# Performance work log

Hardware: AMD Instinct MI355X
Metric: run time of the kernel (lower is better)

## Reference

```python
import jax, jax.numpy as jnp
import numpy as np

D_MODEL = 1024
N_HEADS = 16
HEAD_DIM = D_MODEL // N_HEADS


def setup_inputs() -> dict:
    key = jax.random.key(0)
    kx, kq, kk, kv, ko = jax.random.split(key, 5)
    scale = 1.0 / np.sqrt(D_MODEL)
    x = jax.random.normal(kx, (4, 2048, D_MODEL), dtype=jnp.float32)
    # nn.Linear weights stored as [out, in]; y = x @ W.T
    W_q = jax.random.normal(kq, (D_MODEL, D_MODEL), dtype=jnp.float32) * scale
    W_k = jax.random.normal(kk, (D_MODEL, D_MODEL), dtype=jnp.float32) * scale
    W_v = jax.random.normal(kv, (D_MODEL, D_MODEL), dtype=jnp.float32) * scale
    W_o = jax.random.normal(ko, (D_MODEL, D_MODEL), dtype=jnp.float32) * scale
    return {"x": x, "W_q": W_q, "W_k": W_k, "W_v": W_v, "W_o": W_o}


def reference(x, W_q, W_k, W_v, W_o):
    B, T, C = x.shape
    H, Dh = N_HEADS, HEAD_DIM

    def proj(W):
        return (x @ W.T).reshape(B, T, H, Dh).transpose(0, 2, 1, 3)  # [B,H,T,Dh]

    Q = proj(W_q)
    K = proj(W_q)  # faithful to source bug: K uses W_q, W_k is unused
    V = proj(W_v)

    scores = jnp.einsum('bhqd,bhkd->bhqk', Q, K) / np.sqrt(Dh)
    causal = jnp.tril(jnp.ones((T, T), dtype=bool))
    scores = jnp.where(causal, scores, -jnp.inf)
    attn = jax.nn.softmax(scores, axis=-1)
    out = jnp.einsum('bhqk,bhkd->bhqd', attn, V)
    out = out.transpose(0, 2, 1, 3).reshape(B, T, C)
    return out @ W_o.T
```

## Files before the change

kernel.cpp:

```cpp
#include <hip/hip_runtime.h>
#include <hip/hip_bf16.h>
#include <type_traits>

typedef unsigned short u16;
typedef __attribute__((ext_vector_type(8))) short bf16x8;
typedef __attribute__((ext_vector_type(4))) float f32x4;
typedef __attribute__((ext_vector_type(2))) unsigned int u32x2;

#define B_  4
#define T_  2048
#define C_  1024
#define H_  16
#define DH_ 64
#define M_  (B_*T_)

#define GLDS16(g, l) __builtin_amdgcn_global_load_lds( \
    (const __attribute__((address_space(1))) void*)(g), \
    (__attribute__((address_space(3))) void*)(l), 16, 0, 0)

__device__ __forceinline__ u16 f2b(float f) {
  union { __hip_bfloat16 h; u16 u; } cv;
  cv.h = __float2bfloat16(f);
  return cv.u;
}

__global__ void cast_all_kernel(const float* __restrict__ x,  const float* __restrict__ w0,
                                const float* __restrict__ w1, const float* __restrict__ w2,
                                u16* __restrict__ xo, u16* __restrict__ o0,
                                u16* __restrict__ o1, u16* __restrict__ o2) {
  int bid = blockIdx.x;
  const float* src; u16* dst; int blk;
  if (bid < 8192) { src = x; dst = xo; blk = bid; }
  else {
    int k = bid - 8192, w = k >> 10;
    src = (w == 0) ? w0 : (w == 1) ? w1 : w2;
    dst = (w == 0) ? o0 : (w == 1) ? o1 : o2;
    blk = k & 1023;
  }
  int i = (blk * 256 + threadIdx.x) * 4;
  float4 v = *(const float4*)(src + i);
  unsigned lo = (unsigned)f2b(v.x) | ((unsigned)f2b(v.y) << 16);
  unsigned hi = (unsigned)f2b(v.z) | ((unsigned)f2b(v.w) << 16);
  uint2 p; p.x = lo; p.y = hi;
  *(uint2*)(dst + i) = p;
}

__global__ __launch_bounds__(256) void gemm_bt_kernel(
    const u16* __restrict__ A, const u16* __restrict__ Bm,
    void* __restrict__ Cout, int mode)
{
  constexpr int K = 1024;
  __shared__ __align__(16) u16 As[128 * 64];
  __shared__ __align__(16) u16 Bs[128 * 64];

  const int tid  = threadIdx.x;
  const int wave = tid >> 6, lane = tid & 63;
  const int quad = lane >> 4, l15 = lane & 15;
  const int x7   = l15 & 7;
  const int wm = (wave >> 1) * 64, wn = (wave & 1) * 64;
  const int tm = blockIdx.x * 128, tn = blockIdx.y * 128;

  f32x4 acc[4][4] = {};

  for (int k0 = 0; k0 < K; k0 += 64) {
#pragma unroll
    for (int it = 0; it < 4; it++) {
      int ch  = it * 256 + tid;
      int row = ch >> 3;
      int cc  = (ch & 7) ^ (row & 7);
      GLDS16(A  + (size_t)(tm + row) * K + k0 + cc * 8, &As[(it * 256 + wave * 64) * 8]);
      GLDS16(Bm + (size_t)(tn + row) * K + k0 + cc * 8, &Bs[(it * 256 + wave * 64) * 8]);
    }
    __syncthreads();

#pragma unroll
    for (int ks = 0; ks < 2; ks++) {
      bf16x8 af[4], bfr[4];
#pragma unroll
      for (int t = 0; t < 4; t++) {
        int co = ((ks * 4 + quad) ^ x7) * 8;
        af[t]  = *(const bf16x8*)(&As[(wm + t * 16 + l15) * 64 + co]);
        bfr[t] = *(const bf16x8*)(&Bs[(wn + t * 16 + l15) * 64 + co]);
      }
#pragma unroll
      for (int mt = 0; mt < 4; mt++)
#pragma unroll
        for (int nt = 0; nt < 4; nt++)
          acc[mt][nt] = __builtin_amdgcn_mfma_f32_16x16x32_bf16(af[mt], bfr[nt], acc[mt][nt], 0, 0, 0);
    }
    __syncthreads();
  }

  if (mode == 0) {
    u16* out = (u16*)Cout;
    if (tn < 1024) {
#pragma unroll
      for (int mt = 0; mt < 4; mt++)
#pragma unroll
        for (int nt = 0; nt < 4; nt++)
#pragma unroll
          for (int r = 0; r < 4; r++) {
            int gm = tm + wm + mt * 16 + quad * 4 + r;
            int gn = tn + wn + nt * 16 + l15;
            int b = gm >> 11, t = gm & 2047;
            int h = gn >> 6, d = gn & 63;
            out[((size_t)((b * 16 + h) * 2048 + t) << 6) + d] = f2b(acc[mt][nt][r]);
          }
    } else {
#pragma unroll
      for (int mt = 0; mt < 4; mt++)
#pragma unroll
        for (int nt = 0; nt < 4; nt++) {
          int gm0 = tm + wm + mt * 16 + quad * 4;
          int gn  = tn - 1024 + wn + nt * 16 + l15;
          int b = gm0 >> 11, t0 = gm0 & 2047;
          int h = gn >> 6, d = gn & 63;
          alignas(8) u16 tmp[4];
#pragma unroll
          for (int r = 0; r < 4; r++) tmp[r] = f2b(acc[mt][nt][r]);
          *(ushort4*)(out + 8388608 + (((size_t)(b * 16 + h) * 64 + d) << 11) + t0)
              = *(const ushort4*)tmp;
        }
    }
  } else {
    float* out = (float*)Cout;
#pragma unroll
    for (int mt = 0; mt < 4; mt++)
#pragma unroll
      for (int nt = 0; nt < 4; nt++)
#pragma unroll
        for (int r = 0; r < 4; r++) {
          int gm = tm + wm + mt * 16 + quad * 4 + r;
          int gn = tn + wn + nt * 16 + l15;
          out[(size_t)gm * 1024 + gn] = acc[mt][nt][r];
        }
  }
}

__global__ __launch_bounds__(512, 4) void gemm_bt512_kernel(
    const u16* __restrict__ A, const u16* __restrict__ Bm, float* __restrict__ out)
{
  constexpr int K = 1024;
  __shared__ __align__(16) u16 As[128 * 64];
  __shared__ __align__(16) u16 Bs[128 * 64];

  const int tid  = threadIdx.x;
  const int wave = tid >> 6, lane = tid & 63;
  const int quad = lane >> 4, l15 = lane & 15;
  const int x7   = l15 & 7;
  const int wm = (wave >> 1) * 32, wn = (wave & 1) * 64;
  const int tm = blockIdx.x * 128, tn = blockIdx.y * 128;

  f32x4 acc[2][4] = {};

  for (int k0 = 0; k0 < K; k0 += 64) {
#pragma unroll
    for (int it = 0; it < 2; it++) {
      int ch  = it * 512 + tid;
      int row = ch >> 3;
      int cc  = (ch & 7) ^ (row & 7);
      GLDS16(A  + (size_t)(tm + row) * K + k0 + cc * 8, &As[(it * 512 + wave * 64) * 8]);
      GLDS16(Bm + (size_t)(tn + row) * K + k0 + cc * 8, &Bs[(it * 512 + wave * 64) * 8]);
    }
    __syncthreads();

#pragma unroll
    for (int ks = 0; ks < 2; ks++) {
      bf16x8 af[2], bfr[4];
      int co = ((ks * 4 + quad) ^ x7) * 8;
#pragma unroll
      for (int t = 0; t < 2; t++)
        af[t]  = *(const bf16x8*)(&As[(wm + t * 16 + l15) * 64 + co]);
#pragma unroll
      for (int t = 0; t < 4; t++)
        bfr[t] = *(const bf16x8*)(&Bs[(wn + t * 16 + l15) * 64 + co]);
#pragma unroll
      for (int mt = 0; mt < 2; mt++)
#pragma unroll
        for (int nt = 0; nt < 4; nt++)
          acc[mt][nt] = __builtin_amdgcn_mfma_f32_16x16x32_bf16(af[mt], bfr[nt], acc[mt][nt], 0, 0, 0);
    }
    __syncthreads();
  }

#pragma unroll
  for (int mt = 0; mt < 2; mt++)
#pragma unroll
    for (int nt = 0; nt < 4; nt++)
#pragma unroll
      for (int r = 0; r < 4; r++) {
        int gm = tm + wm + mt * 16 + quad * 4 + r;
        int gn = tn + wn + nt * 16 + l15;
        out[(size_t)gm * 1024 + gn] = acc[mt][nt][r];
      }
}

__global__ __launch_bounds__(256, 4) void attn_kernel(
    const u16* __restrict__ Q, const u16* __restrict__ Vt, u16* __restrict__ AO)
{
  __shared__ __align__(16) u16 Ks[2][4096];
  __shared__ __align__(16) u16 Vs[2][4096];

  const int tid  = threadIdx.x;
  const int wave = tid >> 6, lane = tid & 63;
  const int quad = lane >> 4, l15 = lane & 15;
  const int x7   = l15 & 7;
  const int krow = (l15 & 3) | ((l15 & 4) << 1) | ((l15 & 8) >> 1);
  const int kx7  = krow & 7;
  const int bid  = blockIdx.x;
  const int bh = (bid & 7) * 8 + ((bid >> 3) & 7);
  const int m  = bid >> 6;
  const int i  = (m & 4) ? ((m & 8) ? m - 12 : m + 4) : 15 - m;
  const int b = bh >> 4, h = bh & 15;
  const u16* Qbh = Q  + (size_t)bh * (T_ * DH_);
  const u16* Vbh = Vt + (size_t)bh * (DH_ * T_);
  const int q0w = i * 128 + wave * 32;
  const int kbd = (q0w + 31) >> 6;
  const int nkb = 2 * i + 2;

  const float C1 = 0.18033688f;
  const float C2 = -28.8539008f;
  const bf16x8 ones = { 0x3F80, 0x3F80, 0x3F80, 0x3F80, 0x3F80, 0x3F80, 0x3F80, 0x3F80 };

  f32x4 o[2][4] = {};
  f32x4 lsumv[2] = {};

  auto stage = [&](int kb, int bufi) {
    const int k0 = kb * 64;
#pragma unroll
    for (int it = 0; it < 2; it++) {
      int ch  = it * 256 + tid;
      int row = ch >> 3;
      int cc  = (ch & 7) ^ (row & 7);
      GLDS16(Qbh + (size_t)(k0 + row) * DH_ + cc * 8, &Ks[bufi][(it * 256 + wave * 64) * 8]);
      GLDS16(Vbh + (size_t)row * T_ + k0 + cc * 8,    &Vs[bufi][(it * 256 + wave * 64) * 8]);
    }
  };

  stage(0, 0);

  bf16x8 qf[2][2];
#pragma unroll
  for (int mt = 0; mt < 2; mt++)
#pragma unroll
    for (int ks = 0; ks < 2; ks++)
      qf[mt][ks] = *(const bf16x8*)(Qbh + (size_t)(q0w + mt * 16 + l15) * DH_ + ks * 32 + quad * 8);

  auto tilecomp = [&](int kb, int bufi, auto DIAGC) {
    constexpr bool DIAG = decltype(DIAGC)::value;
    const int k0 = kb * 64;
    const u16* KsB = Ks[bufi];
    const u16* VsB = Vs[bufi];

    f32x4 s[2][4] = {};
#pragma unroll
    for (int ks = 0; ks < 2; ks++)
#pragma unroll
      for (int nt = 0; nt < 4; nt++) {
        bf16x8 kf = *(const bf16x8*)(&KsB[(nt * 16 + krow) * 64 + (((ks * 4 + quad) ^ kx7) * 8)]);
#pragma unroll
        for (int mt = 0; mt < 2; mt++)
          s[mt][nt] = __builtin_amdgcn_mfma_f32_16x16x32_bf16(kf, qf[mt][ks], s[mt][nt], 0, 0, 0);
      }

    unsigned c[2][4][2];
#pragma unroll
    for (int mt = 0; mt < 2; mt++)
#pragma unroll
      for (int nt = 0; nt < 4; nt++) {
        u16 pb[4];
#pragma unroll
        for (int r = 0; r < 4; r++) {
          float p = __builtin_amdgcn_exp2f(s[mt][nt][r] * C1 + C2);
          if constexpr (DIAG) {
            int qg = q0w + mt * 16 + l15;
            int kg = k0 + nt * 16 + (quad & 1) * 8 + (quad >> 1) * 4 + r;
            p = (kg <= qg) ? p : 0.0f;
          }
          pb[r] = f2b(p);
        }
        c[mt][nt][0] = (unsigned)pb[0] | ((unsigned)pb[1] << 16);
        c[mt][nt][1] = (unsigned)pb[2] | ((unsigned)pb[3] << 16);
      }

#pragma unroll
    for (int ks2 = 0; ks2 < 2; ks2++) {
      bf16x8 pf[2];
#pragma unroll
      for (int mt = 0; mt < 2; mt++) {
        u32x2 w02 = __builtin_amdgcn_permlane32_swap(c[mt][2 * ks2][0], c[mt][2 * ks2 + 1][0], false, false);
        u32x2 w13 = __builtin_amdgcn_permlane32_swap(c[mt][2 * ks2][1], c[mt][2 * ks2 + 1][1], false, false);
        union { unsigned u[4]; bf16x8 v; } pk;
        pk.u[0] = w02[0]; pk.u[1] = w13[0]; pk.u[2] = w02[1]; pk.u[3] = w13[1];
        pf[mt] = pk.v;
        lsumv[mt] = __builtin_amdgcn_mfma_f32_16x16x32_bf16(pf[mt], ones, lsumv[mt], 0, 0, 0);
      }
#pragma unroll
      for (int dt = 0; dt < 4; dt++) {
        bf16x8 vf = *(const bf16x8*)(&VsB[(dt * 16 + l15) * 64 + (((ks2 * 4 + quad) ^ x7) * 8)]);
#pragma unroll
        for (int mt = 0; mt < 2; mt++)
          o[mt][dt] = __builtin_amdgcn_mfma_f32_16x16x32_bf16(pf[mt], vf, o[mt][dt], 0, 0, 0);
      }
    }
  };

  for (int kb = 0; kb < nkb; kb++) {
    __syncthreads();
    if (kb + 1 < nkb) stage(kb + 1, (kb + 1) & 1);
    const int bufi = kb & 1;
    if (kb < kbd)        tilecomp(kb, bufi, std::false_type{});
    else if (kb == kbd)  tilecomp(kb, bufi, std::true_type{});
  }

#pragma unroll
  for (int mt = 0; mt < 2; mt++)
#pragma unroll
    for (int r = 0; r < 4; r++) {
      float rl = 1.0f / lsumv[mt][r];
      int t = q0w + mt * 16 + quad * 4 + r;
#pragma unroll
      for (int dt = 0; dt < 4; dt++)
        AO[((size_t)(b * T_ + t)) * C_ + h * DH_ + dt * 16 + l15] = f2b(o[mt][dt][r] * rl);
    }
}

extern "C" void kernel_launch(void* const* d_in, const int* in_sizes, int n_in,
                              void* d_out, int out_size, void* d_ws, size_t ws_size,
                              hipStream_t stream) {
  (void)in_sizes; (void)n_in; (void)out_size; (void)ws_size;
  const float* x  = (const float*)d_in[0];
  const float* Wq = (const float*)d_in[1];
  const float* Wv = (const float*)d_in[3];
  const float* Wo = (const float*)d_in[4];

  u16* Xb  = (u16*)d_ws;
  u16* AOw = Xb;
  u16* Wqb = Xb  + 8388608;
  u16* Wvb = Wqb + 1048576;
  u16* Wob = Wvb + 1048576;
  u16* Qw  = Wob + 1048576;
  u16* Vtw = Qw  + 8388608;

  cast_all_kernel<<<11264, 256, 0, stream>>>(x, Wq, Wv, Wo, Xb, Wqb, Wvb, Wob);

  gemm_bt_kernel<<<dim3(64, 16), 256, 0, stream>>>(Xb, Wqb, (void*)Qw, 0);

  attn_kernel<<<1024, 256, 0, stream>>>(Qw, Vtw, AOw);

  gemm_bt512_kernel<<<dim3(64, 8), 512, 0, stream>>>(AOw, Wob, (float*)d_out);
}
```

Baseline: 210.3 us.

## Replace GEMMs with 256x128-tile multi-buffered pipelined kernel using manual waitcnt

Both projection GEMMs now use one templated kernel with 512 threads and 256x128 output tiles. It triple-buffers the A tile and double-buffers the B tile in LDS, prefetching future K slices with global_load_lds and waiting on partial vmcnt counts, so loads overlap MFMA work instead of hitting a full sync on every iteration. The larger tiles raise operand reuse and halve the block count. The cost is more LDS per block, lower occupancy, and fewer blocks for the output GEMM, which launches only 256.

```diff
diff --git a/kernel.cpp b/kernel.cpp
--- a/kernel.cpp
+++ b/kernel.cpp
@@ -45,53 +45,86 @@
   *(uint2*)(dst + i) = p;
 }
 
-__global__ __launch_bounds__(256) void gemm_bt_kernel(
-    const u16* __restrict__ A, const u16* __restrict__ Bm,
-    void* __restrict__ Cout, int mode)
+template<int MODE>
+__global__ __launch_bounds__(512, 2) void gemm256_kernel(
+    const u16* __restrict__ A, const u16* __restrict__ Bm, void* __restrict__ Cout)
 {
   constexpr int K = 1024;
-  __shared__ __align__(16) u16 As[128 * 64];
-  __shared__ __align__(16) u16 Bs[128 * 64];
+  constexpr int NT = K / 64;
+  __shared__ __align__(16) u16 As[3][256 * 64];
+  __shared__ __align__(16) u16 Bs[2][128 * 64];
 
   const int tid  = threadIdx.x;
   const int wave = tid >> 6, lane = tid & 63;
   const int quad = lane >> 4, l15 = lane & 15;
   const int x7   = l15 & 7;
-  const int wm = (wave >> 1) * 64, wn = (wave & 1) * 64;
-  const int tm = blockIdx.x * 128, tn = blockIdx.y * 128;
+  const int wr = wave >> 1, wc = wave & 1;
+  const int tm = blockIdx.x * 256, tn = blockIdx.y * 128;
 
   f32x4 acc[4][4] = {};
 
-  for (int k0 = 0; k0 < K; k0 += 64) {
+  auto stageA = [&](int t, int bi) {
+    const int k0 = t * 64;
 #pragma unroll
     for (int it = 0; it < 4; it++) {
-      int ch  = it * 256 + tid;
+      int ch  = it * 512 + tid;
       int row = ch >> 3;
       int cc  = (ch & 7) ^ (row & 7);
-      GLDS16(A  + (size_t)(tm + row) * K + k0 + cc * 8, &As[(it * 256 + wave * 64) * 8]);
-      GLDS16(Bm + (size_t)(tn + row) * K + k0 + cc * 8, &Bs[(it * 256 + wave * 64) * 8]);
-    }
-    __syncthreads();
-
-#pragma unroll
-    for (int ks = 0; ks < 2; ks++) {
-      bf16x8 af[4], bfr[4];
-#pragma unroll
-      for (int t = 0; t < 4; t++) {
-        int co = ((ks * 4 + quad) ^ x7) * 8;
-        af[t]  = *(const bf16x8*)(&As[(wm + t * 16 + l15) * 64 + co]);
-        bfr[t] = *(const bf16x8*)(&Bs[(wn + t * 16 + l15) * 64 + co]);
-      }
+      GLDS16(A + (size_t)(tm + row) * K + k0 + cc * 8, &As[bi][(it * 512 + wave * 64) * 8]);
+    }
+  };
+  auto stageB = [&](int t, int bi) {
+    const int k0 = t * 64;
+#pragma unroll
+    for (int it = 0; it < 2; it++) {
+      int ch  = it * 512 + tid;
+      int row = ch >> 3;
+      int cc  = (ch & 7) ^ (row & 7);
+      GLDS16(Bm + (size_t)(tn + row) * K + k0 + cc * 8, &Bs[bi][(it * 512 + wave * 64) * 8]);
+    }
+  };
+
+  stageB(0, 0);
+  stageA(0, 0);
+  stageA(1, 1);
+
+  int bufA = 0, bufAn = 2;
+  for (int t = 0; t < NT; t++) {
+    __builtin_amdgcn_s_barrier();
+    if (t + 1 < NT) stageB(t + 1, (t + 1) & 1);
+    if (t + 2 < NT) { stageA(t + 2, bufAn); bufAn = (bufAn == 2) ? 0 : bufAn + 1; }
+    if (t < NT - 2)       asm volatile("s_waitcnt vmcnt(10)" ::: "memory");
+    else if (t == NT - 2) asm volatile("s_waitcnt vmcnt(6)"  ::: "memory");
+    else                  asm volatile("s_waitcnt vmcnt(0)"  ::: "memory");
+    __builtin_amdgcn_sched_barrier(0);
+    __builtin_amdgcn_s_barrier();
+    __builtin_amdgcn_sched_barrier(0);
+
+    const u16* Ab = &As[bufA][0];
+    const u16* Bb = &Bs[t & 1][0];
+    bufA = (bufA == 2) ? 0 : bufA + 1;
+
+    bf16x8 af[4][2], bfr[4][2];
+#pragma unroll
+    for (int mt = 0; mt < 4; mt++)
+#pragma unroll
+      for (int ks = 0; ks < 2; ks++)
+        af[mt][ks] = *(const bf16x8*)(&Ab[(wr * 64 + mt * 16 + l15) * 64 + (((ks * 4 + quad) ^ x7) * 8)]);
+#pragma unroll
+    for (int nt = 0; nt < 4; nt++)
+#pragma unroll
+      for (int ks = 0; ks < 2; ks++)
+        bfr[nt][ks] = *(const bf16x8*)(&Bb[(wc * 64 + nt * 16 + l15) * 64 + (((ks * 4 + quad) ^ x7) * 8)]);
+#pragma unroll
+    for (int ks = 0; ks < 2; ks++)
 #pragma unroll
       for (int mt = 0; mt < 4; mt++)
 #pragma unroll
         for (int nt = 0; nt < 4; nt++)
-          acc[mt][nt] = __builtin_amdgcn_mfma_f32_16x16x32_bf16(af[mt], bfr[nt], acc[mt][nt], 0, 0, 0);
-    }
-    __syncthreads();
+          acc[mt][nt] = __builtin_amdgcn_mfma_f32_16x16x32_bf16(af[mt][ks], bfr[nt][ks], acc[mt][nt], 0, 0, 0);
   }
 
-  if (mode == 0) {
+  if constexpr (MODE == 0) {
     u16* out = (u16*)Cout;
     if (tn < 1024) {
 #pragma unroll
@@ -100,8 +133,8 @@
         for (int nt = 0; nt < 4; nt++)
 #pragma unroll
           for (int r = 0; r < 4; r++) {
-            int gm = tm + wm + mt * 16 + quad * 4 + r;
-            int gn = tn + wn + nt * 16 + l15;
+            int gm = tm + wr * 64 + mt * 16 + quad * 4 + r;
+            int gn = tn + wc * 64 + nt * 16 + l15;
             int b = gm >> 11, t = gm & 2047;
             int h = gn >> 6, d = gn & 63;
             out[((size_t)((b * 16 + h) * 2048 + t) << 6) + d] = f2b(acc[mt][nt][r]);
@@ -111,8 +144,8 @@
       for (int mt = 0; mt < 4; mt++)
 #pragma unroll
         for (int nt = 0; nt < 4; nt++) {
-          int gm0 = tm + wm + mt * 16 + quad * 4;
-          int gn  = tn - 1024 + wn + nt * 16 + l15;
+          int gm0 = tm + wr * 64 + mt * 16 + quad * 4;
+          int gn  = tn - 1024 + wc * 64 + nt * 16 + l15;
           int b = gm0 >> 11, t0 = gm0 & 2047;
           int h = gn >> 6, d = gn & 63;
           alignas(8) u16 tmp[4];
@@ -130,69 +163,11 @@
       for (int nt = 0; nt < 4; nt++)
 #pragma unroll
         for (int r = 0; r < 4; r++) {
-          int gm = tm + wm + mt * 16 + quad * 4 + r;
-          int gn = tn + wn + nt * 16 + l15;
+          int gm = tm + wr * 64 + mt * 16 + quad * 4 + r;
+          int gn = tn + wc * 64 + nt * 16 + l15;
           out[(size_t)gm * 1024 + gn] = acc[mt][nt][r];
         }
   }
-}
-
-__global__ __launch_bounds__(512, 4) void gemm_bt512_kernel(
-    const u16* __restrict__ A, const u16* __restrict__ Bm, float* __restrict__ out)
-{
-  constexpr int K = 1024;
-  __shared__ __align__(16) u16 As[128 * 64];
-  __shared__ __align__(16) u16 Bs[128 * 64];
-
-  const int tid  = threadIdx.x;
-  const int wave = tid >> 6, lane = tid & 63;
-  const int quad = lane >> 4, l15 = lane & 15;
-  const int x7   = l15 & 7;
-  const int wm = (wave >> 1) * 32, wn = (wave & 1) * 64;
-  const int tm = blockIdx.x * 128, tn = blockIdx.y * 128;
-
-  f32x4 acc[2][4] = {};
-
-  for (int k0 = 0; k0 < K; k0 += 64) {
-#pragma unroll
-    for (int it = 0; it < 2; it++) {
-      int ch  = it * 512 + tid;
-      int row = ch >> 3;
-      int cc  = (ch & 7) ^ (row & 7);
-      GLDS16(A  + (size_t)(tm + row) * K + k0 + cc * 8, &As[(it * 512 + wave * 64) * 8]);
-      GLDS16(Bm + (size_t)(tn + row) * K + k0 + cc * 8, &Bs[(it * 512 + wave * 64) * 8]);
-    }
-    __syncthreads();
-
-#pragma unroll
-    for (int ks = 0; ks < 2; ks++) {
-      bf16x8 af[2], bfr[4];
-      int co = ((ks * 4 + quad) ^ x7) * 8;
-#pragma unroll
-      for (int t = 0; t < 2; t++)
-        af[t]  = *(const bf16x8*)(&As[(wm + t * 16 + l15) * 64 + co]);
-#pragma unroll
-      for (int t = 0; t < 4; t++)
-        bfr[t] = *(const bf16x8*)(&Bs[(wn + t * 16 + l15) * 64 + co]);
-#pragma unroll
-      for (int mt = 0; mt < 2; mt++)
-#pragma unroll
-        for (int nt = 0; nt < 4; nt++)
-          acc[mt][nt] = __builtin_amdgcn_mfma_f32_16x16x32_bf16(af[mt], bfr[nt], acc[mt][nt], 0, 0, 0);
-    }
-    __syncthreads();
-  }
-
-#pragma unroll
-  for (int mt = 0; mt < 2; mt++)
-#pragma unroll
-    for (int nt = 0; nt < 4; nt++)
-#pragma unroll
-      for (int r = 0; r < 4; r++) {
-        int gm = tm + wm + mt * 16 + quad * 4 + r;
-        int gn = tn + wn + nt * 16 + l15;
-        out[(size_t)gm * 1024 + gn] = acc[mt][nt][r];
-      }
 }
 
 __global__ __launch_bounds__(256, 4) void attn_kernel(
@@ -344,9 +319,9 @@
 
   cast_all_kernel<<<11264, 256, 0, stream>>>(x, Wq, Wv, Wo, Xb, Wqb, Wvb, Wob);
 
-  gemm_bt_kernel<<<dim3(64, 16), 256, 0, stream>>>(Xb, Wqb, (void*)Qw, 0);
+  gemm256_kernel<0><<<dim3(32, 16), 512, 0, stream>>>(Xb, Wqb, (void*)Qw);
 
   attn_kernel<<<1024, 256, 0, stream>>>(Qw, Vtw, AOw);
 
-  gemm_bt512_kernel<<<dim3(64, 8), 512, 0, stream>>>(AOw, Wob, (float*)d_out);
-}
+  gemm256_kernel<1><<<dim3(32, 8), 512, 0, stream>>>(AOw, Wob, (void*)d_out);
+}
```

Result: faster. 201.4 us (-4.2%).
